# Kernel tuning notes

Measured on AMD Instinct MI355X. Metric: run time of the kernel, lower is better.

The kernel has to match this reference:

```python
import jax, jax.numpy as jnp
import numpy as np
import itertools


def _identity_grid(n, d, h, w, dtype):
    # Replicates AffineGridGenerator with identity theta:
    # linspace(-1,1,K) per axis (align_corners=True convention),
    # grid[..., 0]=x(W), grid[...,1]=y(H), grid[...,2]=z(D).
    zs = jnp.linspace(-1.0, 1.0, d, dtype=dtype) if d > 1 else jnp.array([-1.0], dtype=dtype)
    ys = jnp.linspace(-1.0, 1.0, h, dtype=dtype) if h > 1 else jnp.array([-1.0], dtype=dtype)
    xs = jnp.linspace(-1.0, 1.0, w, dtype=dtype) if w > 1 else jnp.array([-1.0], dtype=dtype)
    gz, gy, gx = jnp.meshgrid(zs, ys, xs, indexing='ij')  # [D,H,W]
    grid = jnp.stack([gx, gy, gz], axis=-1)               # [D,H,W,3]
    return jnp.broadcast_to(grid, (n, d, h, w, 3))


def _trilinear_sample(x, grid):
    N, C, Din, Hin, Win = x.shape
    dt = x.dtype
    fx = (grid[..., 0] + 1.0) * 0.5 * (Win - 1)
    fy = (grid[..., 1] + 1.0) * 0.5 * (Hin - 1)
    fz = (grid[..., 2] + 1.0) * 0.5 * (Din - 1)
    x0 = jnp.floor(fx); y0 = jnp.floor(fy); z0 = jnp.floor(fz)
    wx1 = (fx - x0).astype(dt); wy1 = (fy - y0).astype(dt); wz1 = (fz - z0).astype(dt)
    wx = (1.0 - wx1, wx1); wy = (1.0 - wy1, wy1); wz = (1.0 - wz1, wz1)
    ix = (x0.astype(jnp.int32), x0.astype(jnp.int32) + 1)
    iy = (y0.astype(jnp.int32), y0.astype(jnp.int32) + 1)
    iz = (z0.astype(jnp.int32), z0.astype(jnp.int32) + 1)

    def gather(xb, izb, iyb, ixb):
        return xb[:, izb, iyb, ixb]  # [C,D,H,W]
    gather_b = jax.vmap(gather)

    out = jnp.zeros((N, C) + grid.shape[1:4], dtype=dt)
    for a, b, c in itertools.product((0, 1), repeat=3):  # (z,y,x) corner
        zi, yi, xi = iz[a], iy[b], ix[c]
        valid = ((zi >= 0) & (zi < Din) & (yi >= 0) & (yi < Hin)
                 & (xi >= 0) & (xi < Win))
        zi = jnp.clip(zi, 0, Din - 1)
        yi = jnp.clip(yi, 0, Hin - 1)
        xi = jnp.clip(xi, 0, Win - 1)
        wgt = (wz[a] * wy[b] * wx[c]) * valid.astype(dt)  # [N,D,H,W]
        vals = gather_b(x, zi, yi, xi)                     # [N,C,D,H,W]
        out = out + vals * wgt[:, None]
    return out


def reference(x, d_out, h_out, w_out, variance):
    if variance:
        x = jnp.exp(x / 2.0)
    grid = _identity_grid(x.shape[0], d_out, h_out, w_out, x.dtype)
    out = _trilinear_sample(x, grid)
    if variance:
        out = jnp.log(out) * 2.0
    return out


def setup_inputs() -> dict:
    key = jax.random.key(0)
    x = jax.random.normal(key, (8, 32, 32, 64, 64), dtype=jnp.float32)
    return {"x": x, "d_out": 48, "h_out": 96, "w_out": 96, "variance": 1}
```

## Files before the change

### kernel.cpp

```cpp
#include <hip/hip_runtime.h>

constexpr int N = 8, C = 32, Din = 32, Hin = 64, Win = 64;
constexpr int Do = 48, Ho = 96, Wo = 96;

constexpr int BLOCK   = 256;
constexpr int NBLOCKS = N * C * Do;
constexpr int GPAD    = 68;
constexpr int F2PAD   = 68;
constexpr int HROWS   = 48;
constexpr int QUADS   = HROWS * (Wo / 4);

typedef float f32x4 __attribute__((ext_vector_type(4)));

__global__ __launch_bounds__(BLOCK, 5)
void resample3d_var_kernel(const float* __restrict__ in, float* __restrict__ out) {
    __shared__ float G[Hin][GPAD];
    __shared__ float F2[HROWS][F2PAD];

    const int tid = threadIdx.x;
    const int bid = blockIdx.x;
    const int zo  = bid % Do;
    const int nc  = bid / Do;

    float fz  = (float)(zo * (Din - 1)) * (1.0f / (float)(Do - 1));
    int   z0  = (int)fz;
    float wz1 = fz - (float)z0;
    int   z1  = min(z0 + 1, Din - 1);
    float wz0 = 1.0f - wz1;

    const float* __restrict__ p0 = in + ((size_t)nc * Din + z0) * (Hin * Win);
    const float* __restrict__ p1 = in + ((size_t)nc * Din + z1) * (Hin * Win);

    constexpr float HALF_LOG2E = 0.7213475204444817f;
    constexpr float TWO_LN2    = 1.3862943611198906f;

    {
        const int sy = tid >> 4;
        const int sx = (tid & 15) << 2;
#pragma unroll
        for (int k = 0; k < 4; ++k) {
            int y = sy + k * 16;
            const float4 a = *reinterpret_cast<const float4*>(p0 + y * Win + sx);
            const float4 b = *reinterpret_cast<const float4*>(p1 + y * Win + sx);
            float4 g;
            g.x = wz0 * __builtin_amdgcn_exp2f(a.x * HALF_LOG2E) + wz1 * __builtin_amdgcn_exp2f(b.x * HALF_LOG2E);
            g.y = wz0 * __builtin_amdgcn_exp2f(a.y * HALF_LOG2E) + wz1 * __builtin_amdgcn_exp2f(b.y * HALF_LOG2E);
            g.z = wz0 * __builtin_amdgcn_exp2f(a.z * HALF_LOG2E) + wz1 * __builtin_amdgcn_exp2f(b.z * HALF_LOG2E);
            g.w = wz0 * __builtin_amdgcn_exp2f(a.w * HALF_LOG2E) + wz1 * __builtin_amdgcn_exp2f(b.w * HALF_LOG2E);
            *reinterpret_cast<float4*>(&G[y][sx]) = g;
        }
    }
    __syncthreads();

    int   x0r[3][4];
    float wxr[3][4];
    {
        int q0 = tid % 24;
        int q1 = q0 + 16; if (q1 >= 24) q1 -= 24;
        int q2 = q0 + 8;  if (q2 >= 24) q2 -= 24;
        int qs[3] = {q0, q1, q2};
#pragma unroll
        for (int p = 0; p < 3; ++p) {
#pragma unroll
            for (int i = 0; i < 4; ++i) {
                int   xo = qs[p] * 4 + i;
                float fx = (float)(xo * (Win - 1)) * (1.0f / (float)(Wo - 1));
                int   x0 = (int)fx;
                x0r[p][i] = x0;
                wxr[p][i] = fx - (float)x0;
            }
        }
    }

    const size_t obase = ((size_t)nc * Do + zo) * (size_t)(Ho * Wo);

#pragma unroll
    for (int h = 0; h < 2; ++h) {
        {
            const int xc = (tid & 15) << 2;
            const int r0 = tid >> 4;
#pragma unroll
            for (int j = 0; j < 3; ++j) {
                int   r   = r0 + 16 * j;
                int   yo  = h * HROWS + r;
                float fy  = (float)(yo * (Hin - 1)) * (1.0f / (float)(Ho - 1));
                int   y0  = (int)fy;
                float wy1 = fy - (float)y0;
                int   y1  = min(y0 + 1, Hin - 1);
                f32x4 g0 = *reinterpret_cast<const f32x4*>(&G[y0][xc]);
                f32x4 g1 = *reinterpret_cast<const f32x4*>(&G[y1][xc]);
                f32x4 f  = g0 + wy1 * (g1 - g0);
                *reinterpret_cast<f32x4*>(&F2[r][xc]) = f;
                if (xc == 60) F2[r][64] = f.w;
            }
        }
        __syncthreads();

        float* __restrict__ ob = out + obase + (size_t)h * (HROWS * Wo);
#pragma unroll
        for (int k = 0; k < 5; ++k) {
            int c = k * BLOCK + tid;
            if (c < QUADS) {
                int row = (c * 2731) >> 16;
                const float* __restrict__ rp = &F2[row][0];
                f32x4 o;
#pragma unroll
                for (int i = 0; i < 4; ++i) {
                    int   x0  = x0r[k % 3][i];
                    float wx1 = wxr[k % 3][i];
                    float F0 = rp[x0], F1 = rp[x0 + 1];
                    o[i] = TWO_LN2 * __log2f(F0 + wx1 * (F1 - F0));
                }
                *reinterpret_cast<f32x4*>(ob + (size_t)c * 4) = o;
            }
        }
        if (h == 0) __syncthreads();
    }
}

extern "C" void kernel_launch(void* const* d_in, const int* in_sizes, int n_in,
                              void* d_out, int out_size, void* d_ws, size_t ws_size,
                              hipStream_t stream) {
    const float* x = (const float*)d_in[0];
    float* out = (float*)d_out;
    resample3d_var_kernel<<<NBLOCKS, BLOCK, 0, stream>>>(x, out);
}
```

Measured before the change: 123.7 us.

## Process four output planes per block with register-prefetched input slabs

Each block now handles four consecutive output depth planes instead of one. While the current plane is being resampled, the global loads for the next plane's two input z-slices are issued into registers, so load latency overlaps with compute. This also amortizes per-block setup such as the x-weight tables. In exchange the grid has a quarter as many blocks, register pressure rises (launch bounds lowered from 5 to 4), and each plane now needs an extra barrier.

```diff
diff --git a/kernel.cpp b/kernel.cpp
--- a/kernel.cpp
+++ b/kernel.cpp
@@ -4,7 +4,8 @@
 constexpr int Do = 48, Ho = 96, Wo = 96;
 
 constexpr int BLOCK   = 256;
-constexpr int NBLOCKS = N * C * Do;
+constexpr int PPB     = 4;
+constexpr int NBLOCKS = N * C * Do / PPB;
 constexpr int GPAD    = 68;
 constexpr int F2PAD   = 68;
 constexpr int HROWS   = 48;
@@ -12,45 +13,41 @@
 
 typedef float f32x4 __attribute__((ext_vector_type(4)));
 
-__global__ __launch_bounds__(BLOCK, 5)
+__global__ __launch_bounds__(BLOCK, 4)
 void resample3d_var_kernel(const float* __restrict__ in, float* __restrict__ out) {
     __shared__ float G[Hin][GPAD];
     __shared__ float F2[HROWS][F2PAD];
 
-    const int tid = threadIdx.x;
-    const int bid = blockIdx.x;
-    const int zo  = bid % Do;
-    const int nc  = bid / Do;
+    const int tid    = threadIdx.x;
+    const int plane0 = blockIdx.x * PPB;
+    const int nc     = plane0 / Do;
+    const int zo0    = plane0 % Do;
 
-    float fz  = (float)(zo * (Din - 1)) * (1.0f / (float)(Do - 1));
-    int   z0  = (int)fz;
-    float wz1 = fz - (float)z0;
-    int   z1  = min(z0 + 1, Din - 1);
-    float wz0 = 1.0f - wz1;
-
-    const float* __restrict__ p0 = in + ((size_t)nc * Din + z0) * (Hin * Win);
-    const float* __restrict__ p1 = in + ((size_t)nc * Din + z1) * (Hin * Win);
+    const float* __restrict__ base = in + (size_t)nc * (Din * Hin * Win);
 
     constexpr float HALF_LOG2E = 0.7213475204444817f;
     constexpr float TWO_LN2    = 1.3862943611198906f;
 
-    {
-        const int sy = tid >> 4;
-        const int sx = (tid & 15) << 2;
-#pragma unroll
-        for (int k = 0; k < 4; ++k) {
-            int y = sy + k * 16;
-            const float4 a = *reinterpret_cast<const float4*>(p0 + y * Win + sx);
-            const float4 b = *reinterpret_cast<const float4*>(p1 + y * Win + sx);
-            float4 g;
-            g.x = wz0 * __builtin_amdgcn_exp2f(a.x * HALF_LOG2E) + wz1 * __builtin_amdgcn_exp2f(b.x * HALF_LOG2E);
-            g.y = wz0 * __builtin_amdgcn_exp2f(a.y * HALF_LOG2E) + wz1 * __builtin_amdgcn_exp2f(b.y * HALF_LOG2E);
-            g.z = wz0 * __builtin_amdgcn_exp2f(a.z * HALF_LOG2E) + wz1 * __builtin_amdgcn_exp2f(b.z * HALF_LOG2E);
-            g.w = wz0 * __builtin_amdgcn_exp2f(a.w * HALF_LOG2E) + wz1 * __builtin_amdgcn_exp2f(b.w * HALF_LOG2E);
-            *reinterpret_cast<float4*>(&G[y][sx]) = g;
-        }
+    const int sy = tid >> 4;
+    const int sx = (tid & 15) << 2;
+
+    f32x4 ra[4], rb[4];
+
+#define ISSUE_LOADS(zovar)                                               \
+    {                                                                    \
+        int   zz  = (zovar);                                             \
+        float fzl = (float)(zz * (Din - 1)) * (1.0f / (float)(Do - 1));  \
+        int   z0l = (int)fzl;                                            \
+        int   z1l = min(z0l + 1, Din - 1);                               \
+        const float* __restrict__ p0 = base + (size_t)z0l * (Hin * Win); \
+        const float* __restrict__ p1 = base + (size_t)z1l * (Hin * Win); \
+        _Pragma("unroll")                                                \
+        for (int k = 0; k < 4; ++k) {                                    \
+            int y = sy + k * 16;                                         \
+            ra[k] = *reinterpret_cast<const f32x4*>(p0 + y * Win + sx);  \
+            rb[k] = *reinterpret_cast<const f32x4*>(p1 + y * Win + sx);  \
+        }                                                                \
     }
-    __syncthreads();
 
     int   x0r[3][4];
     float wxr[3][4];
@@ -72,50 +69,72 @@
         }
     }
 
-    const size_t obase = ((size_t)nc * Do + zo) * (size_t)(Ho * Wo);
+    ISSUE_LOADS(zo0)
+
+    for (int j = 0; j < PPB; ++j) {
+        const int zo = zo0 + j;
+        float fz  = (float)(zo * (Din - 1)) * (1.0f / (float)(Do - 1));
+        float wz1 = fz - (float)(int)fz;
+        float wz0 = 1.0f - wz1;
 
 #pragma unroll
-    for (int h = 0; h < 2; ++h) {
-        {
-            const int xc = (tid & 15) << 2;
-            const int r0 = tid >> 4;
+        for (int k = 0; k < 4; ++k) {
+            int y = sy + k * 16;
+            f32x4 g;
 #pragma unroll
-            for (int j = 0; j < 3; ++j) {
-                int   r   = r0 + 16 * j;
-                int   yo  = h * HROWS + r;
-                float fy  = (float)(yo * (Hin - 1)) * (1.0f / (float)(Ho - 1));
-                int   y0  = (int)fy;
-                float wy1 = fy - (float)y0;
-                int   y1  = min(y0 + 1, Hin - 1);
-                f32x4 g0 = *reinterpret_cast<const f32x4*>(&G[y0][xc]);
-                f32x4 g1 = *reinterpret_cast<const f32x4*>(&G[y1][xc]);
-                f32x4 f  = g0 + wy1 * (g1 - g0);
-                *reinterpret_cast<f32x4*>(&F2[r][xc]) = f;
-                if (xc == 60) F2[r][64] = f.w;
-            }
+            for (int i = 0; i < 4; ++i)
+                g[i] = wz0 * __builtin_amdgcn_exp2f(ra[k][i] * HALF_LOG2E)
+                     + wz1 * __builtin_amdgcn_exp2f(rb[k][i] * HALF_LOG2E);
+            *reinterpret_cast<f32x4*>(&G[y][sx]) = g;
         }
         __syncthreads();
 
-        float* __restrict__ ob = out + obase + (size_t)h * (HROWS * Wo);
+        if (j + 1 < PPB) ISSUE_LOADS(zo + 1)
+
+        const size_t obase = ((size_t)nc * Do + zo) * (size_t)(Ho * Wo);
+
 #pragma unroll
-        for (int k = 0; k < 5; ++k) {
-            int c = k * BLOCK + tid;
-            if (c < QUADS) {
-                int row = (c * 2731) >> 16;
-                const float* __restrict__ rp = &F2[row][0];
-                f32x4 o;
+        for (int h = 0; h < 2; ++h) {
+            {
 #pragma unroll
-                for (int i = 0; i < 4; ++i) {
-                    int   x0  = x0r[k % 3][i];
-                    float wx1 = wxr[k % 3][i];
-                    float F0 = rp[x0], F1 = rp[x0 + 1];
-                    o[i] = TWO_LN2 * __log2f(F0 + wx1 * (F1 - F0));
+                for (int jj = 0; jj < 3; ++jj) {
+                    int   r   = sy + 16 * jj;
+                    int   yo  = h * HROWS + r;
+                    float fy  = (float)(yo * (Hin - 1)) * (1.0f / (float)(Ho - 1));
+                    int   y0  = (int)fy;
+                    float wy1 = fy - (float)y0;
+                    int   y1  = min(y0 + 1, Hin - 1);
+                    f32x4 g0 = *reinterpret_cast<const f32x4*>(&G[y0][sx]);
+                    f32x4 g1 = *reinterpret_cast<const f32x4*>(&G[y1][sx]);
+                    f32x4 f  = g0 + wy1 * (g1 - g0);
+                    *reinterpret_cast<f32x4*>(&F2[r][sx]) = f;
+                    if (sx == 60) F2[r][64] = f.w;
                 }
-                *reinterpret_cast<f32x4*>(ob + (size_t)c * 4) = o;
             }
+            __syncthreads();
+
+            float* __restrict__ ob = out + obase + (size_t)h * (HROWS * Wo);
+#pragma unroll
+            for (int k = 0; k < 5; ++k) {
+                int c = k * BLOCK + tid;
+                if (c < QUADS) {
+                    int row = (c * 2731) >> 16;
+                    const float* __restrict__ rp = &F2[row][0];
+                    f32x4 o;
+#pragma unroll
+                    for (int i = 0; i < 4; ++i) {
+                        int   x0  = x0r[k % 3][i];
+                        float wx1 = wxr[k % 3][i];
+                        float F0 = rp[x0], F1 = rp[x0 + 1];
+                        o[i] = TWO_LN2 * __log2f(F0 + wx1 * (F1 - F0));
+                    }
+                    *reinterpret_cast<f32x4*>(ob + (size_t)c * 4) = o;
+                }
+            }
+            __syncthreads();
         }
-        if (h == 0) __syncthreads();
     }
+#undef ISSUE_LOADS
 }
 
 extern "C" void kernel_launch(void* const* d_in, const int* in_sizes, int n_in,
```

Result: slower. 149.9 us (+21.2%).
